# Performance work log

Measured on AMD Instinct MI355X. Metric: run time of the kernel, lower is better.

The kernel has to match this reference:

```python
import jax, jax.numpy as jnp
import numpy as np

MIN_POS = 1e-6
EPS = 1e-20
B, S, F_IN, E, H = 2, 1024, 768, 768, 12
DH = E // H   # nnmf in_features per head (64)
FH = E // H   # nnmf out_features per head (hidden_features=embed_dim default)
N_NNMF_ITERS = 3
N_ALPHA_ITERS = 3


def l1norm(x, axis=-1):
    # F.normalize(x, p=1, dim=axis, eps=1e-20) for non-negative x
    return x / jnp.maximum(jnp.sum(jnp.abs(x), axis=axis, keepdims=True), EPS)


def setup_inputs() -> dict:
    key = jax.random.key(0)
    k = jax.random.split(key, 6)
    return {
        "x": jax.random.normal(k[0], (B, S, F_IN), jnp.float32),
        "embed_w": jax.random.normal(k[1], (E, F_IN), jnp.float32) * 0.02,
        "embed_b": jnp.zeros((E,), jnp.float32),
        "nnmf_w": jax.random.uniform(k[2], (FH, DH), jnp.float32),  # non-negative NMF dictionary
        "out_w": jax.random.normal(k[3], (F_IN, E), jnp.float32) * 0.02,
        "out_b": jnp.zeros((F_IN,), jnp.float32),
    }


def reference(x, embed_w, embed_b, nnmf_w, out_w, out_b):
    # normalize NMF weight rows (p=1 over in_features), as nnmf_layer.normalize_weights
    W = nnmf_w / jnp.maximum(jnp.sum(nnmf_w, axis=1, keepdims=True), EPS)  # [FH, DH]

    # embed + clamp positive, split heads
    xe = jnp.clip(x @ embed_w.T + embed_b, MIN_POS)            # [B,S,E]
    xe = xe.reshape(B, S, H, DH)                                # [B,S,H,DH]

    # NNMFDense: prepared_input = l1-normalized input (normalize_input_dim=-1)
    inp = l1norm(xe)                                            # [B,S,H,DH]
    h = l1norm(jnp.ones((B, S, H, FH), x.dtype))                # init hidden
    rec = inp
    for _ in range(N_NNMF_ITERS):
        rec = l1norm(jnp.clip(h @ W, MIN_POS))                  # reconstruction [B,S,H,DH]
        h = l1norm(jnp.clip(h * ((inp / rec) @ W.T), MIN_POS))  # multiplicative update

    # normalize_h (p=1, dim=-1)
    h = l1norm(h)                                               # [B,S,H,FH] -> 'bohf'

    # alpha dynamics fixed point
    alpha = jnp.ones((B, H, S, S), x.dtype)                     # 'bhoi'
    h_rec_input = rec * inp                                     # [B,S,H,DH]
    for _ in range(N_ALPHA_ITERS):
        h_mixed = jnp.einsum('bohf,bhoi->bihf', h, alpha)       # [B,S,H,FH]
        arec_inv = 1.0 / (h_mixed @ W + EPS)                    # _reconstruct -> [B,S,H,DH]
        alpha = alpha * jnp.einsum('bohf,bihf->bhoi', h_rec_input, arec_inv)

    out = jnp.einsum('bohf,bhoi->bihf', h, alpha)               # [B,S,H,FH]
    out = out.reshape(B, S, E)                                  # flatten heads
    return out @ out_w.T + out_b                                # out_project
```

## Files before the change

### kernel.cpp

```cpp
#include <hip/hip_runtime.h>

#define B_  2
#define S_  1024
#define FIN 768
#define E_  768
#define H_  12
#define DH  64

typedef unsigned int uint;
typedef unsigned short ushort;
typedef __attribute__((ext_vector_type(8))) short short8;
typedef __attribute__((ext_vector_type(4))) float floatx4;

__device__ __forceinline__ ushort f2bf(float f) {
    uint u = __float_as_uint(f);
    return (ushort)((u + 0x7fffu + ((u >> 16) & 1u)) >> 16);
}

__device__ __forceinline__ uint4 pack8(const ushort* p) {
    uint4 r;
    r.x = (uint)p[0] | ((uint)p[1] << 16);
    r.y = (uint)p[2] | ((uint)p[3] << 16);
    r.z = (uint)p[4] | ((uint)p[5] << 16);
    r.w = (uint)p[6] | ((uint)p[7] << 16);
    return r;
}

__device__ __forceinline__ void split8v(float4 a, float4 b, short8& hi, short8& lo) {
    float v[8] = {a.x, a.y, a.z, a.w, b.x, b.y, b.z, b.w};
    ushort h[8], l[8];
#pragma unroll
    for (int j = 0; j < 8; ++j) {
        h[j] = f2bf(v[j]);
        l[j] = f2bf(v[j] - __uint_as_float(((uint)h[j]) << 16));
    }
    uint4 H = pack8(h), L = pack8(l);
    hi = *(short8*)&H;
    lo = *(short8*)&L;
}

__global__ __launch_bounds__(256) void k_embed_prep(const float* __restrict__ xs,
                                                    const float* __restrict__ ew,
                                                    const float* __restrict__ eb,
                                                    const float* __restrict__ nw,
                                                    float* __restrict__ Wn,
                                                    float* __restrict__ WnT,
                                                    float* __restrict__ r1inv,
                                                    float* __restrict__ zbase,
                                                    float* __restrict__ inp) {
    __shared__ __align__(16) unsigned char smem[28160];
    const int tid = threadIdx.x;
    const int bid = blockIdx.x;

    if (bid >= 768) {
        const int pb = bid - 768;
        if (pb == 0) {
            float* Wl = (float*)smem;
            const int f = tid >> 2, q = tid & 3;
            float v[16];
            float s = 0.f;
#pragma unroll
            for (int i = 0; i < 16; ++i) { v[i] = nw[f * 64 + q * 16 + i]; s += v[i]; }
            s += __shfl_xor(s, 1, 64);
            s += __shfl_xor(s, 2, 64);
            const float inv = 1.f / fmaxf(s, 1e-20f);
#pragma unroll
            for (int i = 0; i < 16; ++i) {
                float w = v[i] * inv;
                Wn[f * 64 + q * 16 + i] = w;
                WnT[(q * 16 + i) * 64 + f] = w;
                Wl[f * 65 + q * 16 + i] = w;
            }
            __syncthreads();
            if (tid < 64) {
                float cs = 0.f;
                for (int ff = 0; ff < 64; ++ff) cs += Wl[ff * 65 + tid];
                float t = fmaxf(cs * (1.f / 64.f), 1e-6f);
                float S = t;
#pragma unroll
                for (int m = 1; m < 64; m <<= 1) S += __shfl_xor(S, m, 64);
                S = fmaxf(S, 1e-20f);
                r1inv[tid] = S / t;
            }
        } else {
            const int i = (pb - 1) * 1024 + tid * 4;
            if (i < 26112) {
                float4 z = make_float4(0.f, 0.f, 0.f, 0.f);
                *(float4*)(zbase + i) = z;
            }
        }
        return;
    }

    const int head = bid % 12;
    const int tok0 = (bid / 12) * 32;
    ushort* As_hi = (ushort*)smem;
    ushort* As_lo = As_hi + 32 * 72;
    ushort* Bs_hi = As_lo + 32 * 72;
    ushort* Bs_lo = Bs_hi + 64 * 72;
    float*  RS    = (float*)(Bs_lo + 64 * 72);

    const int wv = tid >> 6, lane = tid & 63;
    const int mbase = (wv >> 1) * 16;
    const int nbase = (wv & 1) * 32;
    const int lm = lane & 15, lq = lane >> 4;

    floatx4 acc[2];
    acc[0] = (floatx4)0.f;
    acc[1] = (floatx4)0.f;

    const int arow = tid >> 3, akc = (tid & 7) * 8;
    const int brow = tid >> 2, bkq = (tid & 3) * 16;
    const float* xrow = xs + (size_t)(tok0 + arow) * FIN + akc;
    const float* wrg  = ew + (size_t)(head * 64 + brow) * FIN + bkq;

    float4 pa[2], pb[4];
#pragma unroll
    for (int c = 0; c < 2; ++c) pa[c] = *(const float4*)(xrow + c * 4);
#pragma unroll
    for (int c = 0; c < 4; ++c) pb[c] = *(const float4*)(wrg + c * 4);

    for (int kb = 0; kb < FIN; kb += 64) {
        __syncthreads();
        {
            ushort ah[8], al[8], bh[16], bl[16];
            float va[8] = {pa[0].x, pa[0].y, pa[0].z, pa[0].w,
                           pa[1].x, pa[1].y, pa[1].z, pa[1].w};
#pragma unroll
            for (int j = 0; j < 8; ++j) {
                ah[j] = f2bf(va[j]);
                al[j] = f2bf(va[j] - __uint_as_float(((uint)ah[j]) << 16));
            }
#pragma unroll
            for (int c4 = 0; c4 < 4; ++c4) {
                float vb[4] = {pb[c4].x, pb[c4].y, pb[c4].z, pb[c4].w};
#pragma unroll
                for (int j = 0; j < 4; ++j) {
                    ushort g = f2bf(vb[j]);
                    bh[c4 * 4 + j] = g;
                    bl[c4 * 4 + j] = f2bf(vb[j] - __uint_as_float(((uint)g) << 16));
                }
            }
            const int aoff = arow * 72 + akc;
            *(uint4*)&As_hi[aoff] = pack8(ah);
            *(uint4*)&As_lo[aoff] = pack8(al);
            const int boff = brow * 72 + bkq;
            *(uint4*)&Bs_hi[boff]     = pack8(bh);
            *(uint4*)&Bs_hi[boff + 8] = pack8(bh + 8);
            *(uint4*)&Bs_lo[boff]     = pack8(bl);
            *(uint4*)&Bs_lo[boff + 8] = pack8(bl + 8);
        }
        __syncthreads();
        if (kb + 64 < FIN) {
#pragma unroll
            for (int c = 0; c < 2; ++c) pa[c] = *(const float4*)(xrow + kb + 64 + c * 4);
#pragma unroll
            for (int c = 0; c < 4; ++c) pb[c] = *(const float4*)(wrg + kb + 64 + c * 4);
        }
#pragma unroll
        for (int ch = 0; ch < 2; ++ch) {
            const int ko = ch * 32 + lq * 8;
            short8 ah = *(const short8*)&As_hi[(mbase + lm) * 72 + ko];
            short8 al = *(const short8*)&As_lo[(mbase + lm) * 72 + ko];
#pragma unroll
            for (int ti = 0; ti < 2; ++ti) {
                short8 bh = *(const short8*)&Bs_hi[(nbase + ti * 16 + lm) * 72 + ko];
                short8 bl = *(const short8*)&Bs_lo[(nbase + ti * 16 + lm) * 72 + ko];
                acc[ti] = __builtin_amdgcn_mfma_f32_16x16x32_bf16(ah, bh, acc[ti], 0, 0, 0);
                acc[ti] = __builtin_amdgcn_mfma_f32_16x16x32_bf16(al, bh, acc[ti], 0, 0, 0);
                acc[ti] = __builtin_amdgcn_mfma_f32_16x16x32_bf16(ah, bl, acc[ti], 0, 0, 0);
            }
        }
    }

    const float b0 = eb[head * 64 + nbase + lm];
    const float b1 = eb[head * 64 + nbase + 16 + lm];
    float xe[2][4];
    float rs[4];
#pragma unroll
    for (int r = 0; r < 4; ++r) {
        float e0 = fmaxf(acc[0][r] + b0, 1e-6f);
        float e1 = fmaxf(acc[1][r] + b1, 1e-6f);
        xe[0][r] = e0; xe[1][r] = e1;
        float p = e0 + e1;
        p += __shfl_xor(p, 1, 64);
        p += __shfl_xor(p, 2, 64);
        p += __shfl_xor(p, 4, 64);
        p += __shfl_xor(p, 8, 64);
        rs[r] = p;
    }
    if (lm == 0) {
#pragma unroll
        for (int r = 0; r < 4; ++r)
            RS[(wv & 1) * 32 + mbase + lq * 4 + r] = rs[r];
    }
    __syncthreads();
    const size_t obase = ((size_t)((tok0 >> 10) * 12 + head) * 1024 + (tok0 & 1023));
#pragma unroll
    for (int r = 0; r < 4; ++r) {
        const int m = mbase + lq * 4 + r;
        const float inv = 1.f / fmaxf(RS[m] + RS[32 + m], 1e-20f);
        float* op = inp + (obase + m) * 64;
        op[nbase + lm]      = xe[0][r] * inv;
        op[nbase + 16 + lm] = xe[1][r] * inv;
    }
}

__device__ __forceinline__ void mfma_matvec(const float srcC[4][4], float* T,
                                            int lm, int lq,
                                            const ushort* WH, const ushort* WL,
                                            floatx4 out[4]) {
    __builtin_amdgcn_wave_barrier();
#pragma unroll
    for (int nt = 0; nt < 4; ++nt)
#pragma unroll
        for (int r = 0; r < 4; ++r)
            T[(lq * 4 + r) * 68 + nt * 16 + lm] = srcC[nt][r];
    __builtin_amdgcn_wave_barrier();
    float4 a00 = *(const float4*)&T[lm * 68 + lq * 8];
    float4 a01 = *(const float4*)&T[lm * 68 + lq * 8 + 4];
    float4 a10 = *(const float4*)&T[lm * 68 + 32 + lq * 8];
    float4 a11 = *(const float4*)&T[lm * 68 + 32 + lq * 8 + 4];
    __builtin_amdgcn_wave_barrier();
    short8 A0h, A0l, A1h, A1l;
    split8v(a00, a01, A0h, A0l);
    split8v(a10, a11, A1h, A1l);
#pragma unroll
    for (int nt = 0; nt < 4; ++nt) {
        const int row = (nt * 16 + lm) * 72;
        short8 b0h = *(const short8*)&WH[row + lq * 8];
        short8 b0l = *(const short8*)&WL[row + lq * 8];
        short8 b1h = *(const short8*)&WH[row + 32 + lq * 8];
        short8 b1l = *(const short8*)&WL[row + 32 + lq * 8];
        floatx4 acc = (floatx4)0.f;
        acc = __builtin_amdgcn_mfma_f32_16x16x32_bf16(A0h, b0h, acc, 0, 0, 0);
        acc = __builtin_amdgcn_mfma_f32_16x16x32_bf16(A0l, b0h, acc, 0, 0, 0);
        acc = __builtin_amdgcn_mfma_f32_16x16x32_bf16(A0h, b0l, acc, 0, 0, 0);
        acc = __builtin_amdgcn_mfma_f32_16x16x32_bf16(A1h, b1h, acc, 0, 0, 0);
        acc = __builtin_amdgcn_mfma_f32_16x16x32_bf16(A1l, b1h, acc, 0, 0, 0);
        acc = __builtin_amdgcn_mfma_f32_16x16x32_bf16(A1h, b1l, acc, 0, 0, 0);
        out[nt] = acc;
    }
}

__global__ __launch_bounds__(256) void k_nnmf(const float* __restrict__ inp,
                                              const float* __restrict__ Wn,
                                              const float* __restrict__ WnT,
                                              const float* __restrict__ r1inv,
                                              float* __restrict__ hout,
                                              float* __restrict__ hriout,
                                              float* __restrict__ mp0) {
    __shared__ ushort WtH[64 * 72], WtL[64 * 72];
    __shared__ ushort WwH[64 * 72], WwL[64 * 72];
    __shared__ float Tb[4][16 * 68];
    const int tid = threadIdx.x, wv = tid >> 6, lane = tid & 63;
    const int lm = lane & 15, lq = lane >> 4;
    float* T = Tb[wv];
    const int rowbase = blockIdx.x * 64 + wv * 16;

    {
        const int row = tid >> 2, kq = (tid & 3) * 16;
        short8 h0, l0, h1, l1;
        split8v(*(const float4*)(WnT + row * 64 + kq), *(const float4*)(WnT + row * 64 + kq + 4), h0, l0);
        split8v(*(const float4*)(WnT + row * 64 + kq + 8), *(const float4*)(WnT + row * 64 + kq + 12), h1, l1);
        *(short8*)&WtH[row * 72 + kq] = h0; *(short8*)&WtH[row * 72 + kq + 8] = h1;
        *(short8*)&WtL[row * 72 + kq] = l0; *(short8*)&WtL[row * 72 + kq + 8] = l1;
        split8v(*(const float4*)(Wn + row * 64 + kq), *(const float4*)(Wn + row * 64 + kq + 4), h0, l0);
        split8v(*(const float4*)(Wn + row * 64 + kq + 8), *(const float4*)(Wn + row * 64 + kq + 12), h1, l1);
        *(short8*)&WwH[row * 72 + kq] = h0; *(short8*)&WwH[row * 72 + kq + 8] = h1;
        *(short8*)&WwL[row * 72 + kq] = l0; *(short8*)&WwL[row * 72 + kq + 8] = l1;
    }

    float inpC[4][4];
#pragma unroll
    for (int nt = 0; nt < 4; ++nt)
#pragma unroll
        for (int r = 0; r < 4; ++r)
            inpC[nt][r] = inp[(size_t)(rowbase + lq * 4 + r) * 64 + nt * 16 + lm];
    float r1c[4];
#pragma unroll
    for (int nt = 0; nt < 4; ++nt) r1c[nt] = r1inv[nt * 16 + lm];
    __syncthreads();

    float hC[4][4], recC[4][4];
    {
        float qC[4][4];
#pragma unroll
        for (int nt = 0; nt < 4; ++nt)
#pragma unroll
            for (int r = 0; r < 4; ++r) qC[nt][r] = inpC[nt][r] * r1c[nt];
        floatx4 u[4];
        mfma_matvec(qC, T, lm, lq, WwH, WwL, u);
#pragma unroll
        for (int nt = 0; nt < 4; ++nt)
#pragma unroll
            for (int r = 0; r < 4; ++r)
                hC[nt][r] = fmaxf(u[nt][r] * (1.f / 64.f), 1e-6f);
#pragma unroll
        for (int r = 0; r < 4; ++r) {
            float s = (hC[0][r] + hC[1][r]) + (hC[2][r] + hC[3][r]);
            s += __shfl_xor(s, 1, 64); s += __shfl_xor(s, 2, 64);
            s += __shfl_xor(s, 4, 64); s += __shfl_xor(s, 8, 64);
            const float inv = __builtin_amdgcn_rcpf(fmaxf(s, 1e-20f));
#pragma unroll
            for (int nt = 0; nt < 4; ++nt) hC[nt][r] *= inv;
        }
    }
#pragma unroll 1
    for (int it = 0; it < 2; ++it) {
        floatx4 t[4];
        mfma_matvec(hC, T, lm, lq, WtH, WtL, t);
        float tC[4][4], qC[4][4];
#pragma unroll
        for (int nt = 0; nt < 4; ++nt)
#pragma unroll
            for (int r = 0; r < 4; ++r) tC[nt][r] = fmaxf(t[nt][r], 1e-6f);
#pragma unroll
        for (int r = 0; r < 4; ++r) {
            float s = (tC[0][r] + tC[1][r]) + (tC[2][r] + tC[3][r]);
            s += __shfl_xor(s, 1, 64); s += __shfl_xor(s, 2, 64);
            s += __shfl_xor(s, 4, 64); s += __shfl_xor(s, 8, 64);
            s = fmaxf(s, 1e-20f);
            const float invS = __builtin_amdgcn_rcpf(s);
#pragma unroll
            for (int nt = 0; nt < 4; ++nt) {
                recC[nt][r] = tC[nt][r] * invS;
                qC[nt][r] = inpC[nt][r] * s * __builtin_amdgcn_rcpf(tC[nt][r]);
            }
        }
        floatx4 u[4];
        mfma_matvec(qC, T, lm, lq, WwH, WwL, u);
#pragma unroll
        for (int nt = 0; nt < 4; ++nt)
#pragma unroll
            for (int r = 0; r < 4; ++r)
                hC[nt][r] = fmaxf(hC[nt][r] * u[nt][r], 1e-6f);
#pragma unroll
        for (int r = 0; r < 4; ++r) {
            float s = (hC[0][r] + hC[1][r]) + (hC[2][r] + hC[3][r]);
            s += __shfl_xor(s, 1, 64); s += __shfl_xor(s, 2, 64);
            s += __shfl_xor(s, 4, 64); s += __shfl_xor(s, 8, 64);
            const float inv = __builtin_amdgcn_rcpf(fmaxf(s, 1e-20f));
#pragma unroll
            for (int nt = 0; nt < 4; ++nt) hC[nt][r] *= inv;
        }
    }
#pragma unroll
    for (int r = 0; r < 4; ++r) {
        float s = (hC[0][r] + hC[1][r]) + (hC[2][r] + hC[3][r]);
        s += __shfl_xor(s, 1, 64); s += __shfl_xor(s, 2, 64);
        s += __shfl_xor(s, 4, 64); s += __shfl_xor(s, 8, 64);
        const float inv = __builtin_amdgcn_rcpf(fmaxf(s, 1e-20f));
#pragma unroll
        for (int nt = 0; nt < 4; ++nt) hC[nt][r] *= inv;
    }
#pragma unroll
    for (int nt = 0; nt < 4; ++nt)
#pragma unroll
        for (int r = 0; r < 4; ++r) {
            const size_t o = (size_t)(rowbase + lq * 4 + r) * 64 + nt * 16 + lm;
            hout[o] = hC[nt][r];
            hriout[o] = recC[nt][r] * inpC[nt][r];
        }
    float hs[4];
#pragma unroll
    for (int nt = 0; nt < 4; ++nt) {
        float s = (hC[nt][0] + hC[nt][1]) + (hC[nt][2] + hC[nt][3]);
        s += __shfl_xor(s, 16, 64);
        s += __shfl_xor(s, 32, 64);
        hs[nt] = s;
    }
    float mvv = lq == 0 ? hs[0] : lq == 1 ? hs[1] : lq == 2 ? hs[2] : hs[3];
    atomicAdd(&mp0[(size_t)blockIdx.x * 64 + lq * 16 + lm], mvv);
}

__global__ __launch_bounds__(256) void k_alpha_step(const float* __restrict__ hin,
                                                    const float* __restrict__ hri,
                                                    const float* __restrict__ Wn,
                                                    const float* __restrict__ mp_in,
                                                    float* __restrict__ mp_out,
                                                    float* __restrict__ c,
                                                    float* __restrict__ M,
                                                    int it) {
    __shared__ float mred[4][64];
    __shared__ float mv[64];
    __shared__ float vv[64];
    __shared__ float cl[64];
    const int tid = threadIdx.x;
    const int bh = blockIdx.x >> 4;
    const int chunk = blockIdx.x & 15;
    const size_t rowbase = (size_t)bh * 1024 + chunk * 64;

    {
        int f = tid & 63, p = tid >> 6;
        float s = 0.f;
#pragma unroll
        for (int pp = 0; pp < 4; ++pp)
            s += mp_in[((size_t)bh * 16 + p * 4 + pp) * 64 + f];
        mred[p][f] = s;
    }
    __syncthreads();
    if (tid < 64)
        mv[tid] = (mred[0][tid] + mred[1][tid]) + (mred[2][tid] + mred[3][tid]);
    __syncthreads();
    {
        int d = tid & 63, qq = tid >> 6;
        float r = 0.f;
#pragma unroll
        for (int ff = 0; ff < 16; ++ff)
            r = fmaf(mv[qq * 16 + ff], Wn[(size_t)(qq * 16 + ff) * 64 + d], r);
        mred[qq][d] = r;
    }
    __syncthreads();
    if (tid < 64)
        vv[tid] = 1.f / (((mred[0][tid] + mred[1][tid]) + (mred[2][tid] + mred[3][tid])) + 1e-20f);
    __syncthreads();
    {
        int o = tid >> 2, dq = tid & 3;
        const float* rp = hri + (rowbase + o) * 64 + dq * 16;
        float dot = 0.f;
#pragma unroll
        for (int t4 = 0; t4 < 16; t4 += 4) {
            float4 r4 = *(const float4*)(rp + t4);
            dot = fmaf(r4.x, vv[dq * 16 + t4 + 0], dot);
            dot = fmaf(r4.y, vv[dq * 16 + t4 + 1], dot);
            dot = fmaf(r4.z, vv[dq * 16 + t4 + 2], dot);
            dot = fmaf(r4.w, vv[dq * 16 + t4 + 3], dot);
        }
        dot += __shfl_xor(dot, 1, 64);
        dot += __shfl_xor(dot, 2, 64);
        float cn = dot;
        if (it >= 2) cn *= c[rowbase + o];
        if (dq == 0) { c[rowbase + o] = cn; cl[o] = cn; }
    }
    __syncthreads();
    {
        const int f4 = (tid & 15) * 4, ogr = tid >> 4;
        float4 a = make_float4(0.f, 0.f, 0.f, 0.f);
#pragma unroll
        for (int oi = 0; oi < 4; ++oi) {
            int o = ogr * 4 + oi;
            float4 h4 = *(const float4*)(hin + (rowbase + o) * 64 + f4);
            float cv = cl[o];
            a.x = fmaf(h4.x, cv, a.x); a.y = fmaf(h4.y, cv, a.y);
            a.z = fmaf(h4.z, cv, a.z); a.w = fmaf(h4.w, cv, a.w);
        }
        a.x += __shfl_xor(a.x, 16, 64); a.y += __shfl_xor(a.y, 16, 64);
        a.z += __shfl_xor(a.z, 16, 64); a.w += __shfl_xor(a.w, 16, 64);
        a.x += __shfl_xor(a.x, 32, 64); a.y += __shfl_xor(a.y, 32, 64);
        a.z += __shfl_xor(a.z, 32, 64); a.w += __shfl_xor(a.w, 32, 64);
        const int w = tid >> 6;
        if ((tid & 63) < 16) *(float4*)&mred[w][(tid & 15) * 4] = a;
    }
    __syncthreads();
    if (tid < 64) {
        float s = (mred[0][tid] + mred[1][tid]) + (mred[2][tid] + mred[3][tid]);
        if (it == 3) atomicAdd(&M[(size_t)bh * 64 + tid], s);
        else mp_out[((size_t)bh * 16 + chunk) * 64 + tid] = s;
    }
}

__global__ __launch_bounds__(256) void k_projbcast(const float* __restrict__ M,
                                                   const float* __restrict__ ow,
                                                   const float* __restrict__ ob,
                                                   float* __restrict__ out) {
    __shared__ float Ml[768];
    __shared__ float ps[4][64];
    __shared__ float yseg[64];
    const int tid = threadIdx.x;
    const int b = blockIdx.x / 192;
    const int rem = blockIdx.x - b * 192;
    const int jt = rem >> 4, rg = rem & 15;
    for (int i = tid; i < 768; i += 256) Ml[i] = M[b * 768 + i];
    __syncthreads();
    const int jj = tid & 63, part = tid >> 6;
    const int j = jt * 64 + jj;
    const float* row = ow + (size_t)j * 768 + part * 192;
    float acc = 0.f;
    for (int t = 0; t < 192; t += 4) {
        float4 w4 = *(const float4*)(row + t);
        acc = fmaf(w4.x, Ml[part * 192 + t + 0], acc);
        acc = fmaf(w4.y, Ml[part * 192 + t + 1], acc);
        acc = fmaf(w4.z, Ml[part * 192 + t + 2], acc);
        acc = fmaf(w4.w, Ml[part * 192 + t + 3], acc);
    }
    ps[part][jj] = acc;
    __syncthreads();
    if (tid < 64)
        yseg[tid] = ps[0][tid] + ps[1][tid] + ps[2][tid] + ps[3][tid] + ob[jt * 64 + tid];
    __syncthreads();
    const int r0 = tid >> 2, c4 = (tid & 3) * 16;
    float4 v4[4];
#pragma unroll
    for (int q = 0; q < 4; ++q) v4[q] = *(const float4*)&yseg[c4 + q * 4];
    float* dst = out + ((size_t)(b * 1024 + rg * 64 + r0)) * 768 + jt * 64 + c4;
#pragma unroll
    for (int q = 0; q < 4; ++q) *(float4*)(dst + q * 4) = v4[q];
}

extern "C" void kernel_launch(void* const* d_in, const int* in_sizes, int n_in,
                              void* d_out, int out_size, void* d_ws, size_t ws_size,
                              hipStream_t stream) {
    const float* xs = (const float*)d_in[0];
    const float* ew = (const float*)d_in[1];
    const float* eb = (const float*)d_in[2];
    const float* nw = (const float*)d_in[3];
    const float* ow = (const float*)d_in[4];
    const float* ob = (const float*)d_in[5];
    float* out = (float*)d_out;

    float* ws    = (float*)d_ws;
    float* inp   = ws;
    float* h     = ws + 1572864;
    float* hri   = ws + 3145728;
    float* Wn    = ws + 4718592;
    float* WnT   = ws + 4722688;
    float* r1inv = ws + 4726784;
    float* mp0   = ws + 4727040;
    float* M     = ws + 4751616;
    float* mp1   = ws + 4753152;
    float* mp2   = ws + 4777728;
    float* c     = ws + 4802304;

    k_embed_prep<<<795, 256, 0, stream>>>(xs, ew, eb, nw, Wn, WnT, r1inv, mp0, inp);
    k_nnmf<<<384, 256, 0, stream>>>(inp, Wn, WnT, r1inv, h, hri, mp0);
    k_alpha_step<<<384, 256, 0, stream>>>(h, hri, Wn, mp0, mp1, c, M, 1);
    k_alpha_step<<<384, 256, 0, stream>>>(h, hri, Wn, mp1, mp2, c, M, 2);
    k_alpha_step<<<384, 256, 0, stream>>>(h, hri, Wn, mp2, mp1, c, M, 3);
    k_projbcast<<<384, 256, 0, stream>>>(M, ow, ob, out);
}
```

Measured before the change: 131.7 us.

## Process two 16-row tiles per wave in NNMF kernel with 128-thread blocks

```diff
diff --git a/kernel.cpp b/kernel.cpp
--- a/kernel.cpp
+++ b/kernel.cpp
@@ -206,25 +206,36 @@
     }
 }
 
-__device__ __forceinline__ void mfma_matvec(const float srcC[4][4], float* T,
-                                            int lm, int lq,
-                                            const ushort* WH, const ushort* WL,
-                                            floatx4 out[4]) {
+__device__ __forceinline__ void mfma_matvec_x2(const float sC[2][4][4],
+                                               float* T0, float* T1,
+                                               int lm, int lq,
+                                               const ushort* WH, const ushort* WL,
+                                               floatx4 out[2][4]) {
     __builtin_amdgcn_wave_barrier();
 #pragma unroll
     for (int nt = 0; nt < 4; ++nt)
 #pragma unroll
-        for (int r = 0; r < 4; ++r)
-            T[(lq * 4 + r) * 68 + nt * 16 + lm] = srcC[nt][r];
+        for (int r = 0; r < 4; ++r) {
+            T0[(lq * 4 + r) * 68 + nt * 16 + lm] = sC[0][nt][r];
+            T1[(lq * 4 + r) * 68 + nt * 16 + lm] = sC[1][nt][r];
+        }
     __builtin_amdgcn_wave_barrier();
-    float4 a00 = *(const float4*)&T[lm * 68 + lq * 8];
-    float4 a01 = *(const float4*)&T[lm * 68 + lq * 8 + 4];
-    float4 a10 = *(const float4*)&T[lm * 68 + 32 + lq * 8];
-    float4 a11 = *(const float4*)&T[lm * 68 + 32 + lq * 8 + 4];
+    float4 a0[2][2], a1[2][2];
+#pragma unroll
+    for (int g = 0; g < 2; ++g) {
+        const float* T = g ? T1 : T0;
+        a0[g][0] = *(const float4*)&T[lm * 68 + lq * 8];
+        a0[g][1] = *(const float4*)&T[lm * 68 + lq * 8 + 4];
+        a1[g][0] = *(const float4*)&T[lm * 68 + 32 + lq * 8];
+        a1[g][1] = *(const float4*)&T[lm * 68 + 32 + lq * 8 + 4];
+    }
     __builtin_amdgcn_wave_barrier();
-    short8 A0h, A0l, A1h, A1l;
-    split8v(a00, a01, A0h, A0l);
-    split8v(a10, a11, A1h, A1l);
+    short8 A0h[2], A0l[2], A1h[2], A1l[2];
+#pragma unroll
+    for (int g = 0; g < 2; ++g) {
+        split8v(a0[g][0], a0[g][1], A0h[g], A0l[g]);
+        split8v(a1[g][0], a1[g][1], A1h[g], A1l[g]);
+    }
 #pragma unroll
     for (int nt = 0; nt < 4; ++nt) {
         const int row = (nt * 16 + lm) * 72;
@@ -232,143 +243,194 @@
         short8 b0l = *(const short8*)&WL[row + lq * 8];
         short8 b1h = *(const short8*)&WH[row + 32 + lq * 8];
         short8 b1l = *(const short8*)&WL[row + 32 + lq * 8];
-        floatx4 acc = (floatx4)0.f;
-        acc = __builtin_amdgcn_mfma_f32_16x16x32_bf16(A0h, b0h, acc, 0, 0, 0);
-        acc = __builtin_amdgcn_mfma_f32_16x16x32_bf16(A0l, b0h, acc, 0, 0, 0);
-        acc = __builtin_amdgcn_mfma_f32_16x16x32_bf16(A0h, b0l, acc, 0, 0, 0);
-        acc = __builtin_amdgcn_mfma_f32_16x16x32_bf16(A1h, b1h, acc, 0, 0, 0);
-        acc = __builtin_amdgcn_mfma_f32_16x16x32_bf16(A1l, b1h, acc, 0, 0, 0);
-        acc = __builtin_amdgcn_mfma_f32_16x16x32_bf16(A1h, b1l, acc, 0, 0, 0);
-        out[nt] = acc;
-    }
-}
-
-__global__ __launch_bounds__(256) void k_nnmf(const float* __restrict__ inp,
-                                              const float* __restrict__ Wn,
-                                              const float* __restrict__ WnT,
-                                              const float* __restrict__ r1inv,
-                                              float* __restrict__ hout,
-                                              float* __restrict__ hriout,
-                                              float* __restrict__ mp0) {
+#pragma unroll
+        for (int g = 0; g < 2; ++g) {
+            floatx4 acc = (floatx4)0.f;
+            acc = __builtin_amdgcn_mfma_f32_16x16x32_bf16(A0h[g], b0h, acc, 0, 0, 0);
+            acc = __builtin_amdgcn_mfma_f32_16x16x32_bf16(A0l[g], b0h, acc, 0, 0, 0);
+            acc = __builtin_amdgcn_mfma_f32_16x16x32_bf16(A0h[g], b0l, acc, 0, 0, 0);
+            acc = __builtin_amdgcn_mfma_f32_16x16x32_bf16(A1h[g], b1h, acc, 0, 0, 0);
+            acc = __builtin_amdgcn_mfma_f32_16x16x32_bf16(A1l[g], b1h, acc, 0, 0, 0);
+            acc = __builtin_amdgcn_mfma_f32_16x16x32_bf16(A1h[g], b1l, acc, 0, 0, 0);
+            out[g][nt] = acc;
+        }
+    }
+}
+
+__global__ __launch_bounds__(128, 1) void k_nnmf(const float* __restrict__ inp,
+                                                 const float* __restrict__ Wn,
+                                                 const float* __restrict__ WnT,
+                                                 const float* __restrict__ r1inv,
+                                                 float* __restrict__ hout,
+                                                 float* __restrict__ hriout,
+                                                 float* __restrict__ mp0) {
     __shared__ ushort WtH[64 * 72], WtL[64 * 72];
     __shared__ ushort WwH[64 * 72], WwL[64 * 72];
-    __shared__ float Tb[4][16 * 68];
+    __shared__ float Tb[2][2][16 * 68];
     const int tid = threadIdx.x, wv = tid >> 6, lane = tid & 63;
     const int lm = lane & 15, lq = lane >> 4;
-    float* T = Tb[wv];
-    const int rowbase = blockIdx.x * 64 + wv * 16;
+    float* T0 = Tb[wv][0];
+    float* T1 = Tb[wv][1];
 
     {
-        const int row = tid >> 2, kq = (tid & 3) * 16;
-        short8 h0, l0, h1, l1;
-        split8v(*(const float4*)(WnT + row * 64 + kq), *(const float4*)(WnT + row * 64 + kq + 4), h0, l0);
-        split8v(*(const float4*)(WnT + row * 64 + kq + 8), *(const float4*)(WnT + row * 64 + kq + 12), h1, l1);
-        *(short8*)&WtH[row * 72 + kq] = h0; *(short8*)&WtH[row * 72 + kq + 8] = h1;
-        *(short8*)&WtL[row * 72 + kq] = l0; *(short8*)&WtL[row * 72 + kq + 8] = l1;
-        split8v(*(const float4*)(Wn + row * 64 + kq), *(const float4*)(Wn + row * 64 + kq + 4), h0, l0);
-        split8v(*(const float4*)(Wn + row * 64 + kq + 8), *(const float4*)(Wn + row * 64 + kq + 12), h1, l1);
-        *(short8*)&WwH[row * 72 + kq] = h0; *(short8*)&WwH[row * 72 + kq + 8] = h1;
-        *(short8*)&WwL[row * 72 + kq] = l0; *(short8*)&WwL[row * 72 + kq + 8] = l1;
-    }
-
-    float inpC[4][4];
+        const int row = tid >> 1, kq = (tid & 1) * 32;
+        short8 h0, l0;
+#pragma unroll
+        for (int hh = 0; hh < 2; ++hh) {
+            const float* src = hh ? Wn : WnT;
+            ushort* dh = hh ? WwH : WtH;
+            ushort* dl = hh ? WwL : WtL;
+#pragma unroll
+            for (int c8 = 0; c8 < 4; ++c8) {
+                split8v(*(const float4*)(src + row * 64 + kq + c8 * 8),
+                        *(const float4*)(src + row * 64 + kq + c8 * 8 + 4), h0, l0);
+                *(short8*)&dh[row * 72 + kq + c8 * 8] = h0;
+                *(short8*)&dl[row * 72 + kq + c8 * 8] = l0;
+            }
+        }
+    }
+
+    const int rb0 = blockIdx.x * 64 + wv * 32;
+    const int rb1 = rb0 + 16;
+    float inpC[2][4][4];
 #pragma unroll
     for (int nt = 0; nt < 4; ++nt)
 #pragma unroll
-        for (int r = 0; r < 4; ++r)
-            inpC[nt][r] = inp[(size_t)(rowbase + lq * 4 + r) * 64 + nt * 16 + lm];
+        for (int r = 0; r < 4; ++r) {
+            inpC[0][nt][r] = inp[(size_t)(rb0 + lq * 4 + r) * 64 + nt * 16 + lm];
+            inpC[1][nt][r] = inp[(size_t)(rb1 + lq * 4 + r) * 64 + nt * 16 + lm];
+        }
     float r1c[4];
 #pragma unroll
     for (int nt = 0; nt < 4; ++nt) r1c[nt] = r1inv[nt * 16 + lm];
     __syncthreads();
 
-    float hC[4][4], recC[4][4];
+    float hC[2][4][4], recC[2][4][4];
     {
-        float qC[4][4];
-#pragma unroll
-        for (int nt = 0; nt < 4; ++nt)
-#pragma unroll
-            for (int r = 0; r < 4; ++r) qC[nt][r] = inpC[nt][r] * r1c[nt];
-        floatx4 u[4];
-        mfma_matvec(qC, T, lm, lq, WwH, WwL, u);
-#pragma unroll
-        for (int nt = 0; nt < 4; ++nt)
-#pragma unroll
-            for (int r = 0; r < 4; ++r)
-                hC[nt][r] = fmaxf(u[nt][r] * (1.f / 64.f), 1e-6f);
+        float qC[2][4][4];
+#pragma unroll
+        for (int g = 0; g < 2; ++g)
+#pragma unroll
+            for (int nt = 0; nt < 4; ++nt)
+#pragma unroll
+                for (int r = 0; r < 4; ++r) qC[g][nt][r] = inpC[g][nt][r] * r1c[nt];
+        floatx4 u[2][4];
+        mfma_matvec_x2(qC, T0, T1, lm, lq, WwH, WwL, u);
+#pragma unroll
+        for (int g = 0; g < 2; ++g)
+#pragma unroll
+            for (int nt = 0; nt < 4; ++nt)
+#pragma unroll
+                for (int r = 0; r < 4; ++r)
+                    hC[g][nt][r] = fmaxf(u[g][nt][r] * (1.f / 64.f), 1e-6f);
 #pragma unroll
         for (int r = 0; r < 4; ++r) {
-            float s = (hC[0][r] + hC[1][r]) + (hC[2][r] + hC[3][r]);
-            s += __shfl_xor(s, 1, 64); s += __shfl_xor(s, 2, 64);
-            s += __shfl_xor(s, 4, 64); s += __shfl_xor(s, 8, 64);
-            const float inv = __builtin_amdgcn_rcpf(fmaxf(s, 1e-20f));
-#pragma unroll
-            for (int nt = 0; nt < 4; ++nt) hC[nt][r] *= inv;
+            float s0 = (hC[0][0][r] + hC[0][1][r]) + (hC[0][2][r] + hC[0][3][r]);
+            float s1 = (hC[1][0][r] + hC[1][1][r]) + (hC[1][2][r] + hC[1][3][r]);
+#pragma unroll
+            for (int m = 1; m < 16; m <<= 1) {
+                s0 += __shfl_xor(s0, m, 64);
+                s1 += __shfl_xor(s1, m, 64);
+            }
+            const float i0 = __builtin_amdgcn_rcpf(fmaxf(s0, 1e-20f));
+            const float i1 = __builtin_amdgcn_rcpf(fmaxf(s1, 1e-20f));
+#pragma unroll
+            for (int nt = 0; nt < 4; ++nt) { hC[0][nt][r] *= i0; hC[1][nt][r] *= i1; }
         }
     }
 #pragma unroll 1
     for (int it = 0; it < 2; ++it) {
-        floatx4 t[4];
-        mfma_matvec(hC, T, lm, lq, WtH, WtL, t);
-        float tC[4][4], qC[4][4];
-#pragma unroll
-        for (int nt = 0; nt < 4; ++nt)
-#pragma unroll
-            for (int r = 0; r < 4; ++r) tC[nt][r] = fmaxf(t[nt][r], 1e-6f);
+        floatx4 t[2][4];
+        mfma_matvec_x2(hC, T0, T1, lm, lq, WtH, WtL, t);
+        float qC[2][4][4];
 #pragma unroll
         for (int r = 0; r < 4; ++r) {
-            float s = (tC[0][r] + tC[1][r]) + (tC[2][r] + tC[3][r]);
-            s += __shfl_xor(s, 1, 64); s += __shfl_xor(s, 2, 64);
-            s += __shfl_xor(s, 4, 64); s += __shfl_xor(s, 8, 64);
-            s = fmaxf(s, 1e-20f);
-            const float invS = __builtin_amdgcn_rcpf(s);
+            float tC0[4], tC1[4];
 #pragma unroll
             for (int nt = 0; nt < 4; ++nt) {
-                recC[nt][r] = tC[nt][r] * invS;
-                qC[nt][r] = inpC[nt][r] * s * __builtin_amdgcn_rcpf(tC[nt][r]);
-            }
-        }
-        floatx4 u[4];
-        mfma_matvec(qC, T, lm, lq, WwH, WwL, u);
-#pragma unroll
-        for (int nt = 0; nt < 4; ++nt)
-#pragma unroll
-            for (int r = 0; r < 4; ++r)
-                hC[nt][r] = fmaxf(hC[nt][r] * u[nt][r], 1e-6f);
+                tC0[nt] = fmaxf(t[0][nt][r], 1e-6f);
+                tC1[nt] = fmaxf(t[1][nt][r], 1e-6f);
+            }
+            float s0 = (tC0[0] + tC0[1]) + (tC0[2] + tC0[3]);
+            float s1 = (tC1[0] + tC1[1]) + (tC1[2] + tC1[3]);
+#pragma unroll
+            for (int m = 1; m < 16; m <<= 1) {
+                s0 += __shfl_xor(s0, m, 64);
+                s1 += __shfl_xor(s1, m, 64);
+            }
+            s0 = fmaxf(s0, 1e-20f);
+            s1 = fmaxf(s1, 1e-20f);
+            const float iS0 = __builtin_amdgcn_rcpf(s0);
+            const float iS1 = __builtin_amdgcn_rcpf(s1);
+#pragma unroll
+            for (int nt = 0; nt < 4; ++nt) {
+                recC[0][nt][r] = tC0[nt] * iS0;
+                recC[1][nt][r] = tC1[nt] * iS1;
+                qC[0][nt][r] = inpC[0][nt][r] * s0 * __builtin_amdgcn_rcpf(tC0[nt]);
+                qC[1][nt][r] = inpC[1][nt][r] * s1 * __builtin_amdgcn_rcpf(tC1[nt]);
+            }
+        }
+        floatx4 u[2][4];
+        mfma_matvec_x2(qC, T0, T1, lm, lq, WwH, WwL, u);
+#pragma unroll
+        for (int g = 0; g < 2; ++g)
+#pragma unroll
+            for (int nt = 0; nt < 4; ++nt)
+#pragma unroll
+                for (int r = 0; r < 4; ++r)
+                    hC[g][nt][r] = fmaxf(hC[g][nt][r] * u[g][nt][r], 1e-6f);
 #pragma unroll
         for (int r = 0; r < 4; ++r) {
-            float s = (hC[0][r] + hC[1][r]) + (hC[2][r] + hC[3][r]);
-            s += __shfl_xor(s, 1, 64); s += __shfl_xor(s, 2, 64);
-            s += __shfl_xor(s, 4, 64); s += __shfl_xor(s, 8, 64);
-            const float inv = __builtin_amdgcn_rcpf(fmaxf(s, 1e-20f));
-#pragma unroll
-            for (int nt = 0; nt < 4; ++nt) hC[nt][r] *= inv;
+            float s0 = (hC[0][0][r] + hC[0][1][r]) + (hC[0][2][r] + hC[0][3][r]);
+            float s1 = (hC[1][0][r] + hC[1][1][r]) + (hC[1][2][r] + hC[1][3][r]);
+#pragma unroll
+            for (int m = 1; m < 16; m <<= 1) {
+                s0 += __shfl_xor(s0, m, 64);
+                s1 += __shfl_xor(s1, m, 64);
+            }
+            const float i0 = __builtin_amdgcn_rcpf(fmaxf(s0, 1e-20f));
+            const float i1 = __builtin_amdgcn_rcpf(fmaxf(s1, 1e-20f));
+#pragma unroll
+            for (int nt = 0; nt < 4; ++nt) { hC[0][nt][r] *= i0; hC[1][nt][r] *= i1; }
         }
     }
 #pragma unroll
     for (int r = 0; r < 4; ++r) {
-        float s = (hC[0][r] + hC[1][r]) + (hC[2][r] + hC[3][r]);
-        s += __shfl_xor(s, 1, 64); s += __shfl_xor(s, 2, 64);
-        s += __shfl_xor(s, 4, 64); s += __shfl_xor(s, 8, 64);
-        const float inv = __builtin_amdgcn_rcpf(fmaxf(s, 1e-20f));
-#pragma unroll
-        for (int nt = 0; nt < 4; ++nt) hC[nt][r] *= inv;
-    }
-#pragma unroll
-    for (int nt = 0; nt < 4; ++nt)
-#pragma unroll
-        for (int r = 0; r < 4; ++r) {
-            const size_t o = (size_t)(rowbase + lq * 4 + r) * 64 + nt * 16 + lm;
-            hout[o] = hC[nt][r];
-            hriout[o] = recC[nt][r] * inpC[nt][r];
-        }
+        float s0 = (hC[0][0][r] + hC[0][1][r]) + (hC[0][2][r] + hC[0][3][r]);
+        float s1 = (hC[1][0][r] + hC[1][1][r]) + (hC[1][2][r] + hC[1][3][r]);
+#pragma unroll
+        for (int m = 1; m < 16; m <<= 1) {
+            s0 += __shfl_xor(s0, m, 64);
+            s1 += __shfl_xor(s1, m, 64);
+        }
+        const float i0 = __builtin_amdgcn_rcpf(fmaxf(s0, 1e-20f));
+        const float i1 = __builtin_amdgcn_rcpf(fmaxf(s1, 1e-20f));
+#pragma unroll
+        for (int nt = 0; nt < 4; ++nt) { hC[0][nt][r] *= i0; hC[1][nt][r] *= i1; }
+    }
     float hs[4];
 #pragma unroll
+    for (int nt = 0; nt < 4; ++nt) hs[nt] = 0.f;
+#pragma unroll
+    for (int g = 0; g < 2; ++g) {
+        const int rb = g ? rb1 : rb0;
+#pragma unroll
+        for (int nt = 0; nt < 4; ++nt) {
+            float gs = 0.f;
+#pragma unroll
+            for (int r = 0; r < 4; ++r) {
+                const size_t o = (size_t)(rb + lq * 4 + r) * 64 + nt * 16 + lm;
+                hout[o] = hC[g][nt][r];
+                hriout[o] = recC[g][nt][r] * inpC[g][nt][r];
+                gs += hC[g][nt][r];
+            }
+            hs[nt] += gs;
+        }
+    }
+#pragma unroll
     for (int nt = 0; nt < 4; ++nt) {
-        float s = (hC[nt][0] + hC[nt][1]) + (hC[nt][2] + hC[nt][3]);
-        s += __shfl_xor(s, 16, 64);
-        s += __shfl_xor(s, 32, 64);
-        hs[nt] = s;
+        hs[nt] += __shfl_xor(hs[nt], 16, 64);
+        hs[nt] += __shfl_xor(hs[nt], 32, 64);
     }
     float mvv = lq == 0 ? hs[0] : lq == 1 ? hs[1] : lq == 2 ? hs[2] : hs[3];
     atomicAdd(&mp0[(size_t)blockIdx.x * 64 + lq * 16 + lm], mvv);
@@ -523,7 +585,7 @@
     float* c     = ws + 4802304;
 
     k_embed_prep<<<795, 256, 0, stream>>>(xs, ew, eb, nw, Wn, WnT, r1inv, mp0, inp);
-    k_nnmf<<<384, 256, 0, stream>>>(inp, Wn, WnT, r1inv, h, hri, mp0);
+    k_nnmf<<<384, 128, 0, stream>>>(inp, Wn, WnT, r1inv, h, hri, mp0);
     k_alpha_step<<<384, 256, 0, stream>>>(h, hri, Wn, mp0, mp1, c, M, 1);
     k_alpha_step<<<384, 256, 0, stream>>>(h, hri, Wn, mp1, mp2, c, M, 2);
     k_alpha_step<<<384, 256, 0, stream>>>(h, hri, Wn, mp2, mp1, c, M, 3);
```

New measurement: 139.8 us. 1.06x slower.
